# Optimization experiments

Measured on AMD Instinct MI355X. Metric: run time of the kernel, lower is better.

The kernel has to match this reference:

```python
import jax, jax.numpy as jnp
import numpy as np


def _slopes(y, x):
    # Finite-difference slopes along the last axis, extended to length N:
    # one-sided at endpoints, averaged in the interior (standard Hermite tangents).
    m = (y[..., 1:] - y[..., :-1]) / (x[1:] - x[:-1])  # [..., N-1]
    return jnp.concatenate(
        [m[..., :1], 0.5 * (m[..., 1:] + m[..., :-1]), m[..., -1:]], axis=-1
    )  # [..., N]


def _interp1d(y, x0, m, xs):
    # y, m: [..., N]; x0: [N] sorted; xs: [Q] queries -> [..., Q]
    I = jnp.searchsorted(x0[1:-1], xs)          # bucket index in [0, N-2]
    x_lo = x0[I]
    dx = x0[I + 1] - x_lo
    t = (xs - x_lo) / dx
    t2 = t * t
    t3 = t2 * t
    h00 = 1.0 - 3.0 * t2 + 2.0 * t3   # A row 0: [1,0,-3,2]
    h10 = t - 2.0 * t2 + t3           # A row 1: [0,1,-2,1]
    h01 = 3.0 * t2 - 2.0 * t3         # A row 2: [0,0,3,-2]
    h11 = t3 - t2                     # A row 3: [0,0,-1,1]
    y_lo = jnp.take(y, I, axis=-1)
    y_hi = jnp.take(y, I + 1, axis=-1)
    m_lo = jnp.take(m, I, axis=-1)
    m_hi = jnp.take(m, I + 1, axis=-1)
    return h00 * y_lo + h10 * m_lo * dx + h01 * y_hi + h11 * m_hi * dx


def setup_inputs() -> dict:
    key = jax.random.key(0)
    k_sig, k_xs, k_ys = jax.random.split(key, 3)
    B, H, W = 32, 512, 512
    Nx, Ny = 1024, 1024
    signal = jax.random.normal(k_sig, (B, H, W), dtype=jnp.float32)
    x1 = jnp.arange(W, dtype=jnp.float32)  # sorted axis for last dim
    x2 = jnp.arange(H, dtype=jnp.float32)  # sorted axis for second-to-last dim
    xs = jnp.sort(jax.random.uniform(k_xs, (Nx,), dtype=jnp.float32) * (W - 1))
    ys = jnp.sort(jax.random.uniform(k_ys, (Ny,), dtype=jnp.float32) * (H - 1))
    return {"signal": signal, "x1": x1, "x2": x2, "xs": xs, "ys": ys}


def reference(signal, x1, x2, xs, ys):
    # Pass 1: interpolate along W at xs -> [B, H, Nx]
    m1 = _slopes(signal, x1)
    out = _interp1d(signal, x1, m1, xs)
    # Pass 2: interpolate along H at ys (operate on transposed data) -> [B, Nx, Ny]
    out_t = jnp.swapaxes(out, -1, -2)   # [B, Nx, H]
    m2 = _slopes(out_t, x2)
    out2 = _interp1d(out_t, x2, m2, ys)
    return jnp.swapaxes(out2, -1, -2)   # [B, Ny, Nx]
```

## Files before the change

kernel.cpp:

```cpp
#include <hip/hip_runtime.h>

#define B_  32
#define H_  512
#define W_  512
#define NX_ 1024
#define NY_ 1024
#define R_  8
#define NB  (H_ / R_)
#define STG (R_ + 3)
#define SW  516
#define MAXQ 64

typedef float f32x4v __attribute__((ext_vector_type(4)));

__device__ __forceinline__ float4 f4mul(float s, float4 a) {
    return make_float4(s * a.x, s * a.y, s * a.z, s * a.w);
}
__device__ __forceinline__ float4 f4fma(float s, float4 a, float4 acc) {
    acc.x += s * a.x; acc.y += s * a.y; acc.z += s * a.z; acc.w += s * a.w;
    return acc;
}

__device__ __forceinline__ void gload_lds16(const float* g, float* l) {
    __builtin_amdgcn_global_load_lds(
        (const __attribute__((address_space(1))) void*)g,
        (__attribute__((address_space(3))) void*)l,
        16, 0, 0);
}

__device__ __forceinline__ void hermite_window(float x, int N, int& c0, float4& v) {
    int i = (int)floorf(x);
    i = min(max(i, 0), N - 2);
    float t  = x - (float)i;
    float t2 = t * t;
    float t3 = t2 * t;
    float h00 = 1.0f - 3.0f * t2 + 2.0f * t3;
    float h10 = t - 2.0f * t2 + t3;
    float h01 = 3.0f * t2 - 2.0f * t3;
    float h11 = t3 - t2;
    if (i == 0) {
        c0 = 0;
        v = make_float4(h00 - h10 - 0.5f * h11, h01 + h10, 0.5f * h11, 0.0f);
    } else if (i == N - 2) {
        c0 = i - 1;
        v = make_float4(-0.5f * h10, h00 - h11, h01 + 0.5f * h10 + h11, 0.0f);
    } else {
        c0 = i - 1;
        v = make_float4(-0.5f * h10, h00 - 0.5f * h11, h01 + 0.5f * h10, 0.5f * h11);
    }
}

__global__ void prep_tables(const float* __restrict__ xs, const float* __restrict__ ys,
                            float4* __restrict__ wxw, int* __restrict__ cx0,
                            float4* __restrict__ wyw, int* __restrict__ ry0,
                            int* __restrict__ bandA, int* __restrict__ bandB) {
    int q = blockIdx.x * blockDim.x + threadIdx.x;
    if (q < NX_) {
        int c; float4 w;
        hermite_window(xs[q], W_, c, w);
        wxw[q] = w; cx0[q] = c;
    } else if (q < NX_ + NY_) {
        int qq = q - NX_;
        int c; float4 w;
        hermite_window(ys[qq], H_, c, w);
        wyw[qq] = w; ry0[qq] = c;
    } else if (q < NX_ + NY_ + 2 * NB) {
        int k = q - NX_ - NY_;
        int isB = (k >= NB) ? 1 : 0;
        int band = k - isB * NB;
        float bound = (float)((band + isB) * R_);
        int lo = 0, hi = NY_;
        while (lo < hi) {
            int m = (lo + hi) >> 1;
            if (ys[m] < bound) lo = m + 1; else hi = m;
        }
        if (isB) bandB[band] = lo; else bandA[band] = lo;
    }
}

__global__ __launch_bounds__(256) void fused(
    const float* __restrict__ sig,
    const float4* __restrict__ wxw, const int* __restrict__ cx0,
    const float4* __restrict__ wyw, const int* __restrict__ ry0,
    const int* __restrict__ bandA, const int* __restrict__ bandB,
    float* __restrict__ out)
{
    __shared__ float stage[STG][SW];
    __shared__ float4 wy_s[MAXQ];
    __shared__ int   slot_s[MAXQ];

    const int tid  = threadIdx.x;
    const int band = blockIdx.x;
    const int b    = blockIdx.y;
    const int r0   = band * R_;

    const int qyA = bandA[band];
    const int nq  = bandB[band] - qyA;

    const float* sb = sig + (size_t)b * H_ * W_;
    float* stf = &stage[0][0];
    #pragma unroll
    for (int it = 0; it < 5; ++it) {
        int j  = it * 256 + tid;
        int s  = j / 129;
        int c4 = j - s * 129;
        int gr = min(max(r0 - 1 + s, 0), H_ - 1);
        int gc = min(c4, 127);
        gload_lds16(sb + (size_t)gr * W_ + gc * 4, stf + (size_t)j * 4);
    }
    if (tid < STG * 129 - 1280) {
        int j  = 1280 + tid;
        int s  = j / 129;
        int c4 = j - s * 129;
        int gr = min(max(r0 - 1 + s, 0), H_ - 1);
        int gc = min(c4, 127);
        *(float4*)(stf + (size_t)j * 4) = ((const float4*)(sb + (size_t)gr * W_))[gc];
    }
    if (tid < nq && tid < MAXQ) {
        int qy = qyA + tid;
        wy_s[tid]   = wyw[qy];
        slot_s[tid] = ry0[qy] - r0 + 1;
    }
    __syncthreads();

    const int qxb = tid * 4;
    const float4 w0 = wxw[qxb], w1 = wxw[qxb + 1], w2 = wxw[qxb + 2], w3 = wxw[qxb + 3];
    const int4 ci = *(const int4*)(cx0 + qxb);
    float4 c[STG];
    #pragma unroll
    for (int s = 0; s < STG; ++s) {
        const float* sr = stage[s];
        c[s].x = w0.x * sr[ci.x] + w0.y * sr[ci.x + 1] + w0.z * sr[ci.x + 2] + w0.w * sr[ci.x + 3];
        c[s].y = w1.x * sr[ci.y] + w1.y * sr[ci.y + 1] + w1.z * sr[ci.y + 2] + w1.w * sr[ci.y + 3];
        c[s].z = w2.x * sr[ci.z] + w2.y * sr[ci.z + 1] + w2.z * sr[ci.z + 2] + w2.w * sr[ci.z + 3];
        c[s].w = w3.x * sr[ci.w] + w3.y * sr[ci.w + 1] + w3.z * sr[ci.w + 2] + w3.w * sr[ci.w + 3];
    }

    float* ob = out + (size_t)b * NY_ * NX_ + qxb;
    for (int j = 0; j < nq; ++j) {
        float4 wv; int s0;
        if (j < MAXQ) { wv = wy_s[j]; s0 = slot_s[j]; }
        else { int qy = qyA + j; wv = wyw[qy]; s0 = ry0[qy] - r0 + 1; }
        s0 = __builtin_amdgcn_readfirstlane(s0);
        float4 acc;
        #define CASE_(S) case S: \
            acc = f4fma(wv.w, c[S + 3], f4fma(wv.z, c[S + 2], \
                  f4fma(wv.y, c[S + 1], f4mul(wv.x, c[S])))); break;
        switch (s0) {
            CASE_(0) CASE_(1) CASE_(2) CASE_(3)
            CASE_(4) CASE_(5) CASE_(6) CASE_(7)
            default: acc = make_float4(0.f, 0.f, 0.f, 0.f); break;
        }
        #undef CASE_
        f32x4v ov = {acc.x, acc.y, acc.z, acc.w};
        __builtin_nontemporal_store(ov, (f32x4v*)(ob + (size_t)(qyA + j) * NX_));
    }
}

extern "C" void kernel_launch(void* const* d_in, const int* in_sizes, int n_in,
                              void* d_out, int out_size, void* d_ws, size_t ws_size,
                              hipStream_t stream) {
    const float* signal = (const float*)d_in[0];
    const float* xs = (const float*)d_in[3];
    const float* ys = (const float*)d_in[4];
    float* out = (float*)d_out;

    float4* wxw = (float4*)d_ws;
    float4* wyw = wxw + NX_;
    int* cx0   = (int*)(wyw + NY_);
    int* ry0   = cx0 + NX_;
    int* bandA = ry0 + NY_;
    int* bandB = bandA + NB;

    prep_tables<<<(NX_ + NY_ + 2 * NB + 255) / 256, 256, 0, stream>>>(
        xs, ys, wxw, cx0, wyw, ry0, bandA, bandB);

    dim3 grid(NB, B_);
    fused<<<grid, 256, 0, stream>>>(signal, wxw, cx0, wyw, ry0, bandA, bandB, out);
}
```

Baseline: 179.3 us.

## Fold table prep into fused kernel and pad LDS rows to avoid bank conflicts

Removes the separate prep_tables launch: each block now computes its own x Hermite weights, y weights and band bounds inline, getting the band bounds from a count-below reduction over ys with shuffles. The LDS staging layout is also changed to insert a 4-float pad after every 32 floats (9 slots per 8 source float4s), so gathered reads at scattered column indices spread across more banks. The aim is to cut the extra kernel launch and the dependency between the two kernels, and to reduce LDS bank conflicts, at the cost of recomputing the weights in every block and one extra barrier.

Result: no change. 179.4 us (+0.0%).

```diff
diff --git a/kernel.cpp b/kernel.cpp
--- a/kernel.cpp
+++ b/kernel.cpp
@@ -8,8 +8,11 @@
 #define R_  8
 #define NB  (H_ / R_)
 #define STG (R_ + 3)
-#define SW  516
 #define MAXQ 64
+
+#define SROW    576
+#define SLOTS_R 144
+#define NSLOT   (STG * SLOTS_R)
 
 typedef float f32x4v __attribute__((ext_vector_type(4)));
 
@@ -50,97 +53,101 @@
     }
 }
 
-__global__ void prep_tables(const float* __restrict__ xs, const float* __restrict__ ys,
-                            float4* __restrict__ wxw, int* __restrict__ cx0,
-                            float4* __restrict__ wyw, int* __restrict__ ry0,
-                            int* __restrict__ bandA, int* __restrict__ bandB) {
-    int q = blockIdx.x * blockDim.x + threadIdx.x;
-    if (q < NX_) {
-        int c; float4 w;
-        hermite_window(xs[q], W_, c, w);
-        wxw[q] = w; cx0[q] = c;
-    } else if (q < NX_ + NY_) {
-        int qq = q - NX_;
-        int c; float4 w;
-        hermite_window(ys[qq], H_, c, w);
-        wyw[qq] = w; ry0[qq] = c;
-    } else if (q < NX_ + NY_ + 2 * NB) {
-        int k = q - NX_ - NY_;
-        int isB = (k >= NB) ? 1 : 0;
-        int band = k - isB * NB;
-        float bound = (float)((band + isB) * R_);
-        int lo = 0, hi = NY_;
-        while (lo < hi) {
-            int m = (lo + hi) >> 1;
-            if (ys[m] < bound) lo = m + 1; else hi = m;
-        }
-        if (isB) bandB[band] = lo; else bandA[band] = lo;
-    }
-}
-
 __global__ __launch_bounds__(256) void fused(
     const float* __restrict__ sig,
-    const float4* __restrict__ wxw, const int* __restrict__ cx0,
-    const float4* __restrict__ wyw, const int* __restrict__ ry0,
-    const int* __restrict__ bandA, const int* __restrict__ bandB,
+    const float* __restrict__ xs,
+    const float* __restrict__ ys,
     float* __restrict__ out)
 {
-    __shared__ float stage[STG][SW];
+    __shared__ float stage[NSLOT * 4];
     __shared__ float4 wy_s[MAXQ];
     __shared__ int   slot_s[MAXQ];
+    __shared__ int   parts[4];
 
     const int tid  = threadIdx.x;
     const int band = blockIdx.x;
     const int b    = blockIdx.y;
     const int r0   = band * R_;
 
-    const int qyA = bandA[band];
-    const int nq  = bandB[band] - qyA;
+    const float* sb = sig + (size_t)b * H_ * W_;
+    float* stf = stage;
+    #pragma unroll
+    for (int it = 0; it < 6; ++it) {
+        int j   = it * 256 + tid;
+        int s   = j / SLOTS_R;
+        int k   = j - s * SLOTS_R;
+        int g   = k / 9;
+        int sub = k - g * 9;
+        int gr  = min(max(r0 - 1 + s, 0), H_ - 1);
+        int idx = min(8 * g + sub, 127);
+        gload_lds16(sb + (size_t)gr * W_ + idx * 4, stf + (size_t)j * 4);
+    }
+    if (tid < NSLOT - 1536) {
+        int j   = 1536 + tid;
+        int s   = j / SLOTS_R;
+        int k   = j - s * SLOTS_R;
+        int g   = k / 9;
+        int sub = k - g * 9;
+        int gr  = min(max(r0 - 1 + s, 0), H_ - 1);
+        int idx = min(8 * g + sub, 127);
+        *(float4*)(stf + (size_t)j * 4) = ((const float4*)(sb + (size_t)gr * W_))[idx];
+    }
 
-    const float* sb = sig + (size_t)b * H_ * W_;
-    float* stf = &stage[0][0];
-    #pragma unroll
-    for (int it = 0; it < 5; ++it) {
-        int j  = it * 256 + tid;
-        int s  = j / 129;
-        int c4 = j - s * 129;
-        int gr = min(max(r0 - 1 + s, 0), H_ - 1);
-        int gc = min(c4, 127);
-        gload_lds16(sb + (size_t)gr * W_ + gc * 4, stf + (size_t)j * 4);
-    }
-    if (tid < STG * 129 - 1280) {
-        int j  = 1280 + tid;
-        int s  = j / 129;
-        int c4 = j - s * 129;
-        int gr = min(max(r0 - 1 + s, 0), H_ - 1);
-        int gc = min(c4, 127);
-        *(float4*)(stf + (size_t)j * 4) = ((const float4*)(sb + (size_t)gr * W_))[gc];
-    }
-    if (tid < nq && tid < MAXQ) {
-        int qy = qyA + tid;
-        wy_s[tid]   = wyw[qy];
-        slot_s[tid] = ry0[qy] - r0 + 1;
+    const int qxb = tid * 4;
+    const float4 xq = *(const float4*)(xs + qxb);
+    int c0a, c0b, c0c, c0d;
+    float4 w0, w1, w2, w3;
+    hermite_window(xq.x, W_, c0a, w0);
+    hermite_window(xq.y, W_, c0b, w1);
+    hermite_window(xq.z, W_, c0c, w2);
+    hermite_window(xq.w, W_, c0d, w3);
+    const int b0 = c0a + ((c0a >> 5) << 2);
+    const int b1 = c0b + ((c0b >> 5) << 2);
+    const int b2 = c0c + ((c0c >> 5) << 2);
+    const int b3 = c0d + ((c0d >> 5) << 2);
+
+    {
+        const float r0f = (float)r0;
+        const float r1f = (float)(r0 + R_);
+        const float4 y4 = *(const float4*)(ys + tid * 4);
+        int clo = (y4.x < r0f) + (y4.y < r0f) + (y4.z < r0f) + (y4.w < r0f);
+        int chi = (y4.x < r1f) + (y4.y < r1f) + (y4.z < r1f) + (y4.w < r1f);
+        int pk = clo | (chi << 16);
+        #pragma unroll
+        for (int d = 32; d; d >>= 1) pk += __shfl_down(pk, d);
+        if ((tid & 63) == 0) parts[tid >> 6] = pk;
     }
     __syncthreads();
 
-    const int qxb = tid * 4;
-    const float4 w0 = wxw[qxb], w1 = wxw[qxb + 1], w2 = wxw[qxb + 2], w3 = wxw[qxb + 3];
-    const int4 ci = *(const int4*)(cx0 + qxb);
+    const int tot = parts[0] + parts[1] + parts[2] + parts[3];
+    const int qyA = tot & 0xFFFF;
+    const int nq  = (tot >> 16) - qyA;
+
     float4 c[STG];
     #pragma unroll
     for (int s = 0; s < STG; ++s) {
-        const float* sr = stage[s];
-        c[s].x = w0.x * sr[ci.x] + w0.y * sr[ci.x + 1] + w0.z * sr[ci.x + 2] + w0.w * sr[ci.x + 3];
-        c[s].y = w1.x * sr[ci.y] + w1.y * sr[ci.y + 1] + w1.z * sr[ci.y + 2] + w1.w * sr[ci.y + 3];
-        c[s].z = w2.x * sr[ci.z] + w2.y * sr[ci.z + 1] + w2.z * sr[ci.z + 2] + w2.w * sr[ci.z + 3];
-        c[s].w = w3.x * sr[ci.w] + w3.y * sr[ci.w + 1] + w3.z * sr[ci.w + 2] + w3.w * sr[ci.w + 3];
+        const float* sr = stf + s * SROW;
+        c[s].x = w0.x * sr[b0] + w0.y * sr[b0 + 1] + w0.z * sr[b0 + 2] + w0.w * sr[b0 + 3];
+        c[s].y = w1.x * sr[b1] + w1.y * sr[b1 + 1] + w1.z * sr[b1 + 2] + w1.w * sr[b1 + 3];
+        c[s].z = w2.x * sr[b2] + w2.y * sr[b2 + 1] + w2.z * sr[b2 + 2] + w2.w * sr[b2 + 3];
+        c[s].w = w3.x * sr[b3] + w3.y * sr[b3 + 1] + w3.z * sr[b3 + 2] + w3.w * sr[b3 + 3];
     }
 
-    float* ob = out + (size_t)b * NY_ * NX_ + qxb;
-    for (int j = 0; j < nq; ++j) {
+    if (tid < nq && tid < MAXQ) {
+        int ry; float4 wv;
+        hermite_window(ys[qyA + tid], H_, ry, wv);
+        wy_s[tid]   = wv;
+        slot_s[tid] = ry - r0 + 1;
+    }
+    __syncthreads();
+
+    float* op = out + (size_t)b * NY_ * NX_ + (size_t)qyA * NX_ + qxb;
+    for (int j = 0; j < nq; ++j, op += NX_) {
         float4 wv; int s0;
         if (j < MAXQ) { wv = wy_s[j]; s0 = slot_s[j]; }
-        else { int qy = qyA + j; wv = wyw[qy]; s0 = ry0[qy] - r0 + 1; }
+        else {
+            int ry; hermite_window(ys[qyA + j], H_, ry, wv); s0 = ry - r0 + 1;
+        }
         s0 = __builtin_amdgcn_readfirstlane(s0);
         float4 acc;
         #define CASE_(S) case S: \
@@ -153,7 +160,7 @@
         }
         #undef CASE_
         f32x4v ov = {acc.x, acc.y, acc.z, acc.w};
-        __builtin_nontemporal_store(ov, (f32x4v*)(ob + (size_t)(qyA + j) * NX_));
+        __builtin_nontemporal_store(ov, (f32x4v*)op);
     }
 }
 
@@ -165,16 +172,6 @@
     const float* ys = (const float*)d_in[4];
     float* out = (float*)d_out;
 
-    float4* wxw = (float4*)d_ws;
-    float4* wyw = wxw + NX_;
-    int* cx0   = (int*)(wyw + NY_);
-    int* ry0   = cx0 + NX_;
-    int* bandA = ry0 + NY_;
-    int* bandB = bandA + NB;
-
-    prep_tables<<<(NX_ + NY_ + 2 * NB + 255) / 256, 256, 0, stream>>>(
-        xs, ys, wxw, cx0, wyw, ry0, bandA, bandB);
-
     dim3 grid(NB, B_);
-    fused<<<grid, 256, 0, stream>>>(signal, wxw, cx0, wyw, ry0, bandA, bandB, out);
+    fused<<<grid, 256, 0, stream>>>(signal, xs, ys, out);
 }
```

## Assign one block per output row and recompute x-pass per row

Applied to the files above, without the earlier changes.

Replaces banded blocks that reuse x-interpolated rows across many y-queries with one block per output row. Each block loads only its 4 input rows into a padded LDS layout and recomputes the x-direction interpolation for them. This removes the band search, the per-query switch and the register-heavy staging, and raises block count and occupancy. The cost is redundant x-pass arithmetic and repeated global/L2 reads of the same input rows.

Result: slower. 209.9 us (+17.1%).

```diff
diff --git a/kernel.cpp b/kernel.cpp
--- a/kernel.cpp
+++ b/kernel.cpp
@@ -5,17 +5,13 @@
 #define W_  512
 #define NX_ 1024
 #define NY_ 1024
-#define R_  8
-#define NB  (H_ / R_)
-#define STG (R_ + 3)
-#define SW  516
-#define MAXQ 64
 
-typedef float f32x4v __attribute__((ext_vector_type(4)));
+#define SLOT_G  17
+#define SLOTS_R 136
+#define SROW    544
+#define NROWS   4
+#define NSLOT   (NROWS * SLOTS_R)
 
-__device__ __forceinline__ float4 f4mul(float s, float4 a) {
-    return make_float4(s * a.x, s * a.y, s * a.z, s * a.w);
-}
 __device__ __forceinline__ float4 f4fma(float s, float4 a, float4 acc) {
     acc.x += s * a.x; acc.y += s * a.y; acc.z += s * a.z; acc.w += s * a.w;
     return acc;
@@ -51,110 +47,81 @@
 }
 
 __global__ void prep_tables(const float* __restrict__ xs, const float* __restrict__ ys,
-                            float4* __restrict__ wxw, int* __restrict__ cx0,
-                            float4* __restrict__ wyw, int* __restrict__ ry0,
-                            int* __restrict__ bandA, int* __restrict__ bandB) {
+                            float4* __restrict__ wxw, int* __restrict__ bx0,
+                            float4* __restrict__ wyw, int* __restrict__ ry0) {
     int q = blockIdx.x * blockDim.x + threadIdx.x;
     if (q < NX_) {
         int c; float4 w;
         hermite_window(xs[q], W_, c, w);
-        wxw[q] = w; cx0[q] = c;
+        wxw[q] = w;
+        bx0[q] = c + ((c >> 6) << 2);
     } else if (q < NX_ + NY_) {
         int qq = q - NX_;
         int c; float4 w;
         hermite_window(ys[qq], H_, c, w);
-        wyw[qq] = w; ry0[qq] = c;
-    } else if (q < NX_ + NY_ + 2 * NB) {
-        int k = q - NX_ - NY_;
-        int isB = (k >= NB) ? 1 : 0;
-        int band = k - isB * NB;
-        float bound = (float)((band + isB) * R_);
-        int lo = 0, hi = NY_;
-        while (lo < hi) {
-            int m = (lo + hi) >> 1;
-            if (ys[m] < bound) lo = m + 1; else hi = m;
-        }
-        if (isB) bandB[band] = lo; else bandA[band] = lo;
+        wyw[qq] = w;
+        ry0[qq] = c;
     }
 }
 
 __global__ __launch_bounds__(256) void fused(
     const float* __restrict__ sig,
-    const float4* __restrict__ wxw, const int* __restrict__ cx0,
+    const float4* __restrict__ wxw, const int* __restrict__ bx0,
     const float4* __restrict__ wyw, const int* __restrict__ ry0,
-    const int* __restrict__ bandA, const int* __restrict__ bandB,
     float* __restrict__ out)
 {
-    __shared__ float stage[STG][SW];
-    __shared__ float4 wy_s[MAXQ];
-    __shared__ int   slot_s[MAXQ];
+    __shared__ float st[NSLOT * 4];
 
-    const int tid  = threadIdx.x;
-    const int band = blockIdx.x;
-    const int b    = blockIdx.y;
-    const int r0   = band * R_;
+    const int tid = threadIdx.x;
+    const int qy  = blockIdx.x;
+    const int b   = blockIdx.y;
 
-    const int qyA = bandA[band];
-    const int nq  = bandB[band] - qyA;
+    const int   ry = ry0[qy];
+    const float4 wy = wyw[qy];
 
     const float* sb = sig + (size_t)b * H_ * W_;
-    float* stf = &stage[0][0];
     #pragma unroll
-    for (int it = 0; it < 5; ++it) {
-        int j  = it * 256 + tid;
-        int s  = j / 129;
-        int c4 = j - s * 129;
-        int gr = min(max(r0 - 1 + s, 0), H_ - 1);
-        int gc = min(c4, 127);
-        gload_lds16(sb + (size_t)gr * W_ + gc * 4, stf + (size_t)j * 4);
+    for (int it = 0; it < 2; ++it) {
+        int j   = it * 256 + tid;
+        int s   = j / SLOTS_R;
+        int k   = j - s * SLOTS_R;
+        int g   = k / SLOT_G;
+        int sub = k - g * SLOT_G;
+        int gr  = min(ry + s, H_ - 1);
+        int idx = min(16 * g + sub, 127);
+        gload_lds16(sb + (size_t)gr * W_ + idx * 4, st + (size_t)j * 4);
     }
-    if (tid < STG * 129 - 1280) {
-        int j  = 1280 + tid;
-        int s  = j / 129;
-        int c4 = j - s * 129;
-        int gr = min(max(r0 - 1 + s, 0), H_ - 1);
-        int gc = min(c4, 127);
-        *(float4*)(stf + (size_t)j * 4) = ((const float4*)(sb + (size_t)gr * W_))[gc];
+    if (tid < NSLOT - 512) {
+        int j   = 512 + tid;
+        int s   = j / SLOTS_R;
+        int k   = j - s * SLOTS_R;
+        int g   = k / SLOT_G;
+        int sub = k - g * SLOT_G;
+        int gr  = min(ry + s, H_ - 1);
+        int idx = min(16 * g + sub, 127);
+        gload_lds16(sb + (size_t)gr * W_ + idx * 4, st + (size_t)j * 4);
     }
-    if (tid < nq && tid < MAXQ) {
-        int qy = qyA + tid;
-        wy_s[tid]   = wyw[qy];
-        slot_s[tid] = ry0[qy] - r0 + 1;
-    }
-    __syncthreads();
 
     const int qxb = tid * 4;
     const float4 w0 = wxw[qxb], w1 = wxw[qxb + 1], w2 = wxw[qxb + 2], w3 = wxw[qxb + 3];
-    const int4 ci = *(const int4*)(cx0 + qxb);
-    float4 c[STG];
+    const int4 bx = *(const int4*)(bx0 + qxb);
+
+    __syncthreads();
+
+    float4 acc = make_float4(0.f, 0.f, 0.f, 0.f);
+    const float wys[4] = {wy.x, wy.y, wy.z, wy.w};
     #pragma unroll
-    for (int s = 0; s < STG; ++s) {
-        const float* sr = stage[s];
-        c[s].x = w0.x * sr[ci.x] + w0.y * sr[ci.x + 1] + w0.z * sr[ci.x + 2] + w0.w * sr[ci.x + 3];
-        c[s].y = w1.x * sr[ci.y] + w1.y * sr[ci.y + 1] + w1.z * sr[ci.y + 2] + w1.w * sr[ci.y + 3];
-        c[s].z = w2.x * sr[ci.z] + w2.y * sr[ci.z + 1] + w2.z * sr[ci.z + 2] + w2.w * sr[ci.z + 3];
-        c[s].w = w3.x * sr[ci.w] + w3.y * sr[ci.w + 1] + w3.z * sr[ci.w + 2] + w3.w * sr[ci.w + 3];
+    for (int s = 0; s < NROWS; ++s) {
+        const float* sr = st + s * SROW;
+        float4 c;
+        c.x = w0.x * sr[bx.x] + w0.y * sr[bx.x + 1] + w0.z * sr[bx.x + 2] + w0.w * sr[bx.x + 3];
+        c.y = w1.x * sr[bx.y] + w1.y * sr[bx.y + 1] + w1.z * sr[bx.y + 2] + w1.w * sr[bx.y + 3];
+        c.z = w2.x * sr[bx.z] + w2.y * sr[bx.z + 1] + w2.z * sr[bx.z + 2] + w2.w * sr[bx.z + 3];
+        c.w = w3.x * sr[bx.w] + w3.y * sr[bx.w + 1] + w3.z * sr[bx.w + 2] + w3.w * sr[bx.w + 3];
+        acc = f4fma(wys[s], c, acc);
     }
 
-    float* ob = out + (size_t)b * NY_ * NX_ + qxb;
-    for (int j = 0; j < nq; ++j) {
-        float4 wv; int s0;
-        if (j < MAXQ) { wv = wy_s[j]; s0 = slot_s[j]; }
-        else { int qy = qyA + j; wv = wyw[qy]; s0 = ry0[qy] - r0 + 1; }
-        s0 = __builtin_amdgcn_readfirstlane(s0);
-        float4 acc;
-        #define CASE_(S) case S: \
-            acc = f4fma(wv.w, c[S + 3], f4fma(wv.z, c[S + 2], \
-                  f4fma(wv.y, c[S + 1], f4mul(wv.x, c[S])))); break;
-        switch (s0) {
-            CASE_(0) CASE_(1) CASE_(2) CASE_(3)
-            CASE_(4) CASE_(5) CASE_(6) CASE_(7)
-            default: acc = make_float4(0.f, 0.f, 0.f, 0.f); break;
-        }
-        #undef CASE_
-        f32x4v ov = {acc.x, acc.y, acc.z, acc.w};
-        __builtin_nontemporal_store(ov, (f32x4v*)(ob + (size_t)(qyA + j) * NX_));
-    }
+    *(float4*)(out + (size_t)b * NY_ * NX_ + (size_t)qy * NX_ + qxb) = acc;
 }
 
 extern "C" void kernel_launch(void* const* d_in, const int* in_sizes, int n_in,
@@ -167,14 +134,12 @@
 
     float4* wxw = (float4*)d_ws;
     float4* wyw = wxw + NX_;
-    int* cx0   = (int*)(wyw + NY_);
-    int* ry0   = cx0 + NX_;
-    int* bandA = ry0 + NY_;
-    int* bandB = bandA + NB;
+    int* bx0 = (int*)(wyw + NY_);
+    int* ry0 = bx0 + NX_;
 
-    prep_tables<<<(NX_ + NY_ + 2 * NB + 255) / 256, 256, 0, stream>>>(
-        xs, ys, wxw, cx0, wyw, ry0, bandA, bandB);
+    prep_tables<<<(NX_ + NY_ + 255) / 256, 256, 0, stream>>>(
+        xs, ys, wxw, bx0, wyw, ry0);
 
-    dim3 grid(NB, B_);
-    fused<<<grid, 256, 0, stream>>>(signal, wxw, cx0, wyw, ry0, bandA, bandB, out);
+    dim3 grid(NY_, B_);
+    fused<<<grid, 256, 0, stream>>>(signal, wxw, bx0, wyw, ry0, out);
 }
```
